# Kernel optimization log

Measured on AMD Instinct MI355X. Metric: run time of the kernel, lower is better.

Reference implementation:

```python
import jax, jax.numpy as jnp
import numpy as np

SCALE = 1.0 / np.sqrt(128.0).astype(np.float32)  # 1/sqrt(head_dim)


def setup_inputs() -> dict:
    key = jax.random.key(0)
    kq, kk, kv = jax.random.split(key, 3)
    B, S, D = 32, 2048, 128
    q = jax.random.normal(kq, (B, S, D), dtype=jnp.float32)
    k = jax.random.normal(kk, (B, S, D), dtype=jnp.float32)
    v = jax.random.normal(kv, (B, S, D), dtype=jnp.float32)
    return {"q": q, "k": k, "v": v}


def reference(q, k, v):
    # attention = bmm(q, k^T) * scale ; softmax over last (key) dim; bmm with v
    scores = jnp.einsum("bsd,btd->bst", q, k) * SCALE  # [B, S, S]
    attn = jax.nn.softmax(scores, axis=-1)
    return jnp.einsum("bst,btd->bsd", attn, v)  # [B, S, D]
```

## Files before the change

### kernel.cpp

```cpp
#include <hip/hip_runtime.h>
#include <math.h>
#include <stdint.h>

typedef __bf16 bf16_t;
typedef __bf16 bf16x2 __attribute__((ext_vector_type(2)));
typedef __bf16 bf16x4 __attribute__((ext_vector_type(4)));
typedef __bf16 bf16x8 __attribute__((ext_vector_type(8)));
typedef float f32x4 __attribute__((ext_vector_type(4)));
typedef float f32x16 __attribute__((ext_vector_type(16)));

#define NB   32
#define SEQ  2048
#define HD   128
#define SCALE 0.08838834764831845f
#define LOG2E 1.4426950408889634f

__device__ __forceinline__ float fast_exp2(float x) {
#if __has_builtin(__builtin_amdgcn_exp2f)
  return __builtin_amdgcn_exp2f(x);
#else
  return exp2f(x);
#endif
}

__global__ __launch_bounds__(256) void prep_kernel(
    const float* __restrict__ Q, const float* __restrict__ K,
    const float* __restrict__ V, bf16_t* __restrict__ Qs,
    bf16_t* __restrict__ Kb, bf16_t* __restrict__ Vt)
{
  const int b = blockIdx.x;
  const int tid = threadIdx.x;
  if (b < 4096) {
    const bool isQ = (b < 2048);
    const float* src = isQ ? Q : K;
    bf16_t* dst = isQ ? Qs : Kb;
    const float sc = isQ ? (SCALE * LOG2E) : 1.0f;
    size_t base4 = (size_t)(isQ ? b : b - 2048) * 1024;
#pragma unroll
    for (int i = 0; i < 4; ++i) {
      size_t idx = base4 + tid + i * 256;
      float4 x = ((const float4*)src)[idx];
      bf16x4 y;
      y[0] = (bf16_t)(x.x * sc); y[1] = (bf16_t)(x.y * sc);
      y[2] = (bf16_t)(x.z * sc); y[3] = (bf16_t)(x.w * sc);
      ((bf16x4*)dst)[idx] = y;
    }
  } else {
    __shared__ float tile[64][65];
    const int bt = b - 4096;
    const int batch = bt >> 6;
    const int rem = bt & 63;
    const int s0 = (rem >> 1) * 64;
    const int d0 = (rem & 1) * 64;
#pragma unroll
    for (int i = 0; i < 4; ++i) {
      int e = tid + i * 256;
      int s = e >> 4, dq = e & 15;
      float4 x = *(const float4*)&V[((size_t)batch * SEQ + s0 + s) * HD + d0 + dq * 4];
      tile[s][dq * 4 + 0] = x.x;
      tile[s][dq * 4 + 1] = x.y;
      tile[s][dq * 4 + 2] = x.z;
      tile[s][dq * 4 + 3] = x.w;
    }
    __syncthreads();
#pragma unroll
    for (int i = 0; i < 2; ++i) {
      int g = tid + i * 256;
      int d = g >> 3, sg = g & 7;
      bf16x8 w;
#pragma unroll
      for (int j = 0; j < 8; ++j) w[j] = (bf16_t)tile[sg * 8 + j][d];
      *(bf16x8*)&Vt[((size_t)batch * HD + d0 + d) * SEQ + s0 + sg * 8] = w;
    }
  }
}

__global__ __launch_bounds__(512, 4) void fa13_kernel(
    const bf16_t* __restrict__ Qs, const bf16_t* __restrict__ Kbf,
    const bf16_t* __restrict__ Vt, float* __restrict__ O)
{
  __shared__ __attribute__((aligned(16))) char smem[68608];
  bf16_t* const Ksw = (bf16_t*)smem;
  bf16_t* const Vsw = (bf16_t*)(smem + 32768);

  const int tid  = threadIdx.x;
  const int lane = tid & 63;
  const int wq   = tid >> 6;
  const int hi   = lane >> 5;
  const int q31  = lane & 31;
  const int pair = wq >> 1;
  const int sub  = wq & 1;
  const int koff = sub * 32;

  const int batch = blockIdx.x >> 4;
  const int qt    = blockIdx.x & 15;

  const bf16_t* Qb = Qs + ((size_t)batch * SEQ + qt * 128 + pair * 32) * HD;
  const bf16_t* Kb = Kbf + (size_t)batch * SEQ * HD;
  const bf16_t* Vb = Vt + (size_t)batch * HD * SEQ;
  float*        Ob = O + ((size_t)batch * SEQ + qt * 128) * HD;

  bf16x8 bq[8];
#pragma unroll
  for (int dc = 0; dc < 8; ++dc)
    bq[dc] = *(const bf16x8*)&Qb[(size_t)q31 * HD + dc * 16 + hi * 8];

  f32x16 o[4];
#pragma unroll
  for (int dt = 0; dt < 4; ++dt)
#pragma unroll
    for (int r = 0; r < 16; ++r) o[dt][r] = 0.f;
  float m_r = -INFINITY, l_r = 0.0f;

  auto stage = [&](int buf, int kb) {
#pragma unroll
    for (int i = 0; i < 2; ++i) {
      int row = wq * 8 + i * 4 + (lane >> 4);
      int gk = (lane & 15) ^ (row & 15);
      const bf16_t* gp = Kb + (size_t)(kb + row) * HD + gk * 8;
      __builtin_amdgcn_global_load_lds(
          (const __attribute__((address_space(1))) void*)gp,
          (__attribute__((address_space(3))) void*)&Ksw[buf * 8192 + (wq * 8 + i * 4) * 128],
          16, 0, 0);
    }
#pragma unroll
    for (int i = 0; i < 2; ++i) {
      int d = wq * 16 + i * 8 + (lane >> 3);
      int gv = (lane & 7) ^ (d & 7);
      const bf16_t* gp = Vb + (size_t)d * SEQ + kb + gv * 8;
      __builtin_amdgcn_global_load_lds(
          (const __attribute__((address_space(1))) void*)gp,
          (__attribute__((address_space(3))) void*)&Vsw[buf * 8192 + (wq * 16 + i * 8) * 64],
          16, 0, 0);
    }
  };

  stage(0, 0);

  for (int t = 0; t < SEQ / 64; ++t) {
    __syncthreads();
    if (t + 1 < SEQ / 64) stage((t + 1) & 1, (t + 1) * 64);

    const bf16_t* Ks = &Ksw[(t & 1) * 8192];
    const bf16_t* Vs = &Vsw[(t & 1) * 8192];

    f32x16 s;
#pragma unroll
    for (int r = 0; r < 16; ++r) s[r] = 0.f;
    {
      const int row = koff + q31;
      const int rsw = row & 15;
#pragma unroll
      for (int dc = 0; dc < 8; ++dc) {
        bf16x8 ak = *(const bf16x8*)&Ks[row * 128 + (((dc * 2 + hi) ^ rsw) * 8)];
        s = __builtin_amdgcn_mfma_f32_32x32x16_bf16(ak, bq[dc], s, 0, 0, 0);
      }
    }

    float mx = s[0];
#pragma unroll
    for (int r = 1; r < 16; ++r) mx = fmaxf(mx, s[r]);
    mx = fmaxf(mx, __shfl_xor(mx, 32));

    if (!__all(mx <= m_r + 8.0f)) {
      const float mnew = fmaxf(m_r, mx);
      const float alpha = fast_exp2(m_r - mnew);
      m_r = mnew;
      l_r *= alpha;
#pragma unroll
      for (int dt = 0; dt < 4; ++dt) o[dt] = o[dt] * alpha;
    }

    float ls = 0.f;
#pragma unroll
    for (int r = 0; r < 16; ++r) {
      float p = fast_exp2(s[r] - m_r);
      s[r] = p; ls += p;
    }
    ls += __shfl_xor(ls, 32);
    l_r += ls;

    uint32_t pk[8];
#pragma unroll
    for (int i = 0; i < 8; ++i) {
      union { bf16x2 v; uint32_t u; } c;
      c.v[0] = (bf16_t)s[2 * i];
      c.v[1] = (bf16_t)s[2 * i + 1];
      pk[i] = c.u;
    }
    uint32_t t0 = __shfl_xor((int)(hi ? pk[0] : pk[2]), 32);
    uint32_t t1 = __shfl_xor((int)(hi ? pk[1] : pk[3]), 32);
    uint32_t t2 = __shfl_xor((int)(hi ? pk[4] : pk[6]), 32);
    uint32_t t3 = __shfl_xor((int)(hi ? pk[5] : pk[7]), 32);
    bf16x8 bp0, bp1;
    {
      union { bf16x8 v; uint32_t w[4]; } B;
      if (hi) { B.w[0] = t0; B.w[1] = t1; B.w[2] = pk[2]; B.w[3] = pk[3]; }
      else    { B.w[0] = pk[0]; B.w[1] = pk[1]; B.w[2] = t0; B.w[3] = t1; }
      bp0 = B.v;
      if (hi) { B.w[0] = t2; B.w[1] = t3; B.w[2] = pk[6]; B.w[3] = pk[7]; }
      else    { B.w[0] = pk[4]; B.w[1] = pk[5]; B.w[2] = t2; B.w[3] = t3; }
      bp1 = B.v;
    }

    {
      const int g0 = (koff >> 3) + hi;
      const int g1 = g0 + 2;
#pragma unroll
      for (int dt = 0; dt < 4; ++dt) {
        const int d = dt * 32 + q31;
        const int dsw = d & 7;
        bf16x8 av0 = *(const bf16x8*)&Vs[d * 64 + ((g0 ^ dsw) * 8)];
        o[dt] = __builtin_amdgcn_mfma_f32_32x32x16_bf16(av0, bp0, o[dt], 0, 0, 0);
        bf16x8 av1 = *(const bf16x8*)&Vs[d * 64 + ((g1 ^ dsw) * 8)];
        o[dt] = __builtin_amdgcn_mfma_f32_32x32x16_bf16(av1, bp1, o[dt], 0, 0, 0);
      }
    }
  }

  __syncthreads();
  float* const sf  = (float*)smem;
  float* const mlb = (float*)(smem + 67584);

  if (sub == 1) {
    if (hi == 0) {
      mlb[pair * 64 + q31]      = m_r;
      mlb[pair * 64 + 32 + q31] = l_r;
    }
#pragma unroll
    for (int dt = 0; dt < 4; ++dt)
#pragma unroll
      for (int r = 0; r < 16; ++r) {
        int d = dt * 32 + (r & 3) + 8 * (r >> 2) + 4 * hi;
        sf[pair * 4224 + q31 * 132 + d] = o[dt][r];
      }
  }
  __syncthreads();
  if (sub == 0) {
    float m1 = mlb[pair * 64 + q31];
    float l1 = mlb[pair * 64 + 32 + q31];
    float m = fmaxf(m_r, m1);
    float e0 = fast_exp2(m_r - m);
    float e1 = fast_exp2(m1 - m);
    float inv = 1.0f / (l_r * e0 + l1 * e1);
    float f0 = e0 * inv, f1 = e1 * inv;
#pragma unroll
    for (int dt = 0; dt < 4; ++dt)
#pragma unroll
      for (int r = 0; r < 16; ++r) {
        int d = dt * 32 + (r & 3) + 8 * (r >> 2) + 4 * hi;
        float* p = &sf[pair * 4224 + q31 * 132 + d];
        *p = o[dt][r] * f0 + *p * f1;
      }
  }
  __syncthreads();
  {
#pragma unroll
    for (int i = 0; i < 8; ++i) {
      int idx = tid + i * 512;
      int q = idx >> 5;
      int dg = idx & 31;
      float4 v = *(const float4*)&sf[(q >> 5) * 4224 + (q & 31) * 132 + dg * 4];
      *(float4*)&Ob[(size_t)q * HD + dg * 4] = v;
    }
  }
}

#define BM   64
#define BN   64
#define KPAD 8
#define VPAD 8
#define PPAD 8

__global__ __launch_bounds__(256) void fa_fallback(
    const float* __restrict__ Q, const float* __restrict__ K,
    const float* __restrict__ V, float* __restrict__ O)
{
  __shared__ __attribute__((aligned(16))) bf16_t Ksh[BN][HD + KPAD];
  __shared__ __attribute__((aligned(16))) bf16_t Vsh[HD][BN + VPAD];
  __shared__ __attribute__((aligned(16))) bf16_t Psh[4][16][BN + PPAD];

  const int tid = threadIdx.x;
  const int lane = tid & 63;
  const int wq = tid >> 6;
  const int quad = lane >> 4;
  const int l15 = lane & 15;
  const int bid = blockIdx.x;
  const int batch = bid >> 5;
  const int qt = bid & 31;

  const float* Qb = Q + (size_t)batch * SEQ * HD + (size_t)qt * BM * HD;
  const float* Kb = K + (size_t)batch * SEQ * HD;
  const float* Vb = V + (size_t)batch * SEQ * HD;
  float* Ob = O + (size_t)batch * SEQ * HD + (size_t)qt * BM * HD;

  bf16x8 aq[4];
  {
    const int qrow = wq * 16 + l15;
#pragma unroll
    for (int kf = 0; kf < 4; ++kf) {
      const float* qp = Qb + (size_t)qrow * HD + kf * 32 + quad * 8;
      float4 x0 = *(const float4*)(qp);
      float4 x1 = *(const float4*)(qp + 4);
      bf16x8 a;
      a[0] = (bf16_t)(x0.x * SCALE); a[1] = (bf16_t)(x0.y * SCALE);
      a[2] = (bf16_t)(x0.z * SCALE); a[3] = (bf16_t)(x0.w * SCALE);
      a[4] = (bf16_t)(x1.x * SCALE); a[5] = (bf16_t)(x1.y * SCALE);
      a[6] = (bf16_t)(x1.z * SCALE); a[7] = (bf16_t)(x1.w * SCALE);
      aq[kf] = a;
    }
  }

  f32x4 o[8];
#pragma unroll
  for (int t = 0; t < 8; ++t) { o[t][0]=0.f; o[t][1]=0.f; o[t][2]=0.f; o[t][3]=0.f; }
  float m_r = -INFINITY, l_r = 0.0f;
  const int vkp = (tid & 31) * 2;
  const int vg = tid >> 5;
  float4 kreg[8], vreg[8];

#pragma unroll
  for (int i = 0; i < 8; ++i) {
    int v = tid + i * 256, row = v >> 5, c4 = (v & 31) * 4;
    kreg[i] = *(const float4*)(Kb + (size_t)row * HD + c4);
  }
#pragma unroll
  for (int i = 0; i < 4; ++i) {
    int d0 = (vg + i * 8) * 4;
    const float* vp0 = Vb + (size_t)vkp * HD + d0;
    vreg[2 * i] = *(const float4*)vp0;
    vreg[2 * i + 1] = *(const float4*)(vp0 + HD);
  }

  for (int kb = 0; kb < SEQ; kb += BN) {
    __syncthreads();
#pragma unroll
    for (int i = 0; i < 8; ++i) {
      int v = tid + i * 256, row = v >> 5, c4 = (v & 31) * 4;
      float4 kv = kreg[i];
      bf16x4 kk;
      kk[0]=(bf16_t)kv.x; kk[1]=(bf16_t)kv.y; kk[2]=(bf16_t)kv.z; kk[3]=(bf16_t)kv.w;
      *(bf16x4*)&Ksh[row][c4] = kk;
    }
#pragma unroll
    for (int i = 0; i < 4; ++i) {
      int d0 = (vg + i * 8) * 4;
      float4 a0 = vreg[2 * i], a1 = vreg[2 * i + 1];
      bf16x2 p0; p0[0]=(bf16_t)a0.x; p0[1]=(bf16_t)a1.x;
      bf16x2 p1; p1[0]=(bf16_t)a0.y; p1[1]=(bf16_t)a1.y;
      bf16x2 p2; p2[0]=(bf16_t)a0.z; p2[1]=(bf16_t)a1.z;
      bf16x2 p3; p3[0]=(bf16_t)a0.w; p3[1]=(bf16_t)a1.w;
      *(bf16x2*)&Vsh[d0 + 0][vkp] = p0;
      *(bf16x2*)&Vsh[d0 + 1][vkp] = p1;
      *(bf16x2*)&Vsh[d0 + 2][vkp] = p2;
      *(bf16x2*)&Vsh[d0 + 3][vkp] = p3;
    }
    __syncthreads();

    const int kbn = kb + BN;
    if (kbn < SEQ) {
#pragma unroll
      for (int i = 0; i < 8; ++i) {
        int v = tid + i * 256, row = v >> 5, c4 = (v & 31) * 4;
        kreg[i] = *(const float4*)(Kb + (size_t)(kbn + row) * HD + c4);
      }
#pragma unroll
      for (int i = 0; i < 4; ++i) {
        int d0 = (vg + i * 8) * 4;
        const float* vp0 = Vb + (size_t)(kbn + vkp) * HD + d0;
        vreg[2 * i] = *(const float4*)vp0;
        vreg[2 * i + 1] = *(const float4*)(vp0 + HD);
      }
    }

    f32x4 s[4];
#pragma unroll
    for (int ct = 0; ct < 4; ++ct) { s[ct][0]=0.f; s[ct][1]=0.f; s[ct][2]=0.f; s[ct][3]=0.f; }
#pragma unroll
    for (int kf = 0; kf < 4; ++kf)
#pragma unroll
      for (int ct = 0; ct < 4; ++ct) {
        bf16x8 ak = *(const bf16x8*)&Ksh[ct * 16 + l15][kf * 32 + quad * 8];
        s[ct] = __builtin_amdgcn_mfma_f32_16x16x32_bf16(ak, aq[kf], s[ct], 0, 0, 0);
      }

    float mx = s[0][0];
#pragma unroll
    for (int ct = 0; ct < 4; ++ct)
#pragma unroll
      for (int r = 0; r < 4; ++r) mx = fmaxf(mx, s[ct][r]);
    mx = fmaxf(mx, __shfl_xor(mx, 16));
    mx = fmaxf(mx, __shfl_xor(mx, 32));
    float mnew = fmaxf(m_r, mx);
    float alpha = __expf(m_r - mnew);
    m_r = mnew;
    float ls = 0.f;
#pragma unroll
    for (int ct = 0; ct < 4; ++ct)
#pragma unroll
      for (int r = 0; r < 4; ++r) {
        float p = __expf(s[ct][r] - mnew);
        s[ct][r] = p; ls += p;
      }
    ls += __shfl_xor(ls, 16);
    ls += __shfl_xor(ls, 32);
    l_r = l_r * alpha + ls;

#pragma unroll
    for (int ct = 0; ct < 4; ++ct) {
      bf16x4 pp;
      pp[0]=(bf16_t)s[ct][0]; pp[1]=(bf16_t)s[ct][1];
      pp[2]=(bf16_t)s[ct][2]; pp[3]=(bf16_t)s[ct][3];
      *(bf16x4*)&Psh[wq][l15][ct * 16 + quad * 4] = pp;
    }
    asm volatile("s_waitcnt lgkmcnt(0)" ::: "memory");
    bf16x8 ap0 = *(const bf16x8*)&Psh[wq][l15][quad * 8];
    bf16x8 ap1 = *(const bf16x8*)&Psh[wq][l15][32 + quad * 8];

#pragma unroll
    for (int t = 0; t < 8; ++t) {
      o[t][0]*=alpha; o[t][1]*=alpha; o[t][2]*=alpha; o[t][3]*=alpha;
    }
#pragma unroll
    for (int t = 0; t < 8; ++t) {
      bf16x8 av0 = *(const bf16x8*)&Vsh[t * 16 + l15][quad * 8];
      o[t] = __builtin_amdgcn_mfma_f32_16x16x32_bf16(av0, ap0, o[t], 0, 0, 0);
      bf16x8 av1 = *(const bf16x8*)&Vsh[t * 16 + l15][32 + quad * 8];
      o[t] = __builtin_amdgcn_mfma_f32_16x16x32_bf16(av1, ap1, o[t], 0, 0, 0);
    }
  }

  float inv = 1.0f / l_r;
  const int qrow = wq * 16 + l15;
#pragma unroll
  for (int t = 0; t < 8; ++t) {
    float4 w;
    w.x = o[t][0]*inv; w.y = o[t][1]*inv; w.z = o[t][2]*inv; w.w = o[t][3]*inv;
    *(float4*)&Ob[(size_t)qrow * HD + t * 16 + quad * 4] = w;
  }
}

extern "C" void kernel_launch(void* const* d_in, const int* in_sizes, int n_in,
                              void* d_out, int out_size, void* d_ws, size_t ws_size,
                              hipStream_t stream) {
  const float* q = (const float*)d_in[0];
  const float* k = (const float*)d_in[1];
  const float* v = (const float*)d_in[2];
  float* out = (float*)d_out;

  const size_t elems = (size_t)NB * SEQ * HD;
  const size_t need = elems * 2 * 3;

  if (ws_size >= need) {
    bf16_t* Qs = (bf16_t*)d_ws;
    bf16_t* Kb = Qs + elems;
    bf16_t* Vt = Kb + elems;
    prep_kernel<<<6144, 256, 0, stream>>>(q, k, v, Qs, Kb, Vt);
    fa13_kernel<<<NB * (SEQ / 128), 512, 0, stream>>>(Qs, Kb, Vt, out);
  } else {
    fa_fallback<<<NB * (SEQ / BM), 256, 0, stream>>>(q, k, v, out);
  }
}
```

Baseline: 270.2 us.

## Software-pipeline PV matmul one tile behind QK with triple-buffered V, smaller blocks

Defers each tile's P·V MFMA to the next iteration so it runs alongside the following tile's Q·K^T, which needs a third V buffer in LDS. Blocks shrink from 512 to 256 threads covering 64 query rows, and each thread now stages twice as many K/V chunks. Block indices are remapped so that consecutive blocks are spread across batches, likely to balance work over XCDs/L2. The aim is to hide the softmax dependency latency and improve MFMA overlap, at the cost of more LDS per block (80KB), which may lower occupancy, and twice the K/V traffic per query row.

```diff
diff --git a/kernel.cpp b/kernel.cpp
--- a/kernel.cpp
+++ b/kernel.cpp
@@ -75,11 +75,11 @@
   }
 }
 
-__global__ __launch_bounds__(512, 4) void fa13_kernel(
+__global__ __launch_bounds__(256) void fa14_kernel(
     const bf16_t* __restrict__ Qs, const bf16_t* __restrict__ Kbf,
     const bf16_t* __restrict__ Vt, float* __restrict__ O)
 {
-  __shared__ __attribute__((aligned(16))) char smem[68608];
+  __shared__ __attribute__((aligned(16))) char smem[81920];
   bf16_t* const Ksw = (bf16_t*)smem;
   bf16_t* const Vsw = (bf16_t*)(smem + 32768);
 
@@ -92,13 +92,14 @@
   const int sub  = wq & 1;
   const int koff = sub * 32;
 
-  const int batch = blockIdx.x >> 4;
-  const int qt    = blockIdx.x & 15;
-
-  const bf16_t* Qb = Qs + ((size_t)batch * SEQ + qt * 128 + pair * 32) * HD;
+  const int L     = ((blockIdx.x & 7) << 7) | (blockIdx.x >> 3);
+  const int batch = L >> 5;
+  const int qt    = L & 31;
+
+  const bf16_t* Qb = Qs + ((size_t)batch * SEQ + qt * 64 + pair * 32) * HD;
   const bf16_t* Kb = Kbf + (size_t)batch * SEQ * HD;
   const bf16_t* Vb = Vt + (size_t)batch * HD * SEQ;
-  float*        Ob = O + ((size_t)batch * SEQ + qt * 128) * HD;
+  float*        Ob = O + ((size_t)batch * SEQ + qt * 64) * HD;
 
   bf16x8 bq[8];
 #pragma unroll
@@ -112,37 +113,40 @@
     for (int r = 0; r < 16; ++r) o[dt][r] = 0.f;
   float m_r = -INFINITY, l_r = 0.0f;
 
-  auto stage = [&](int buf, int kb) {
-#pragma unroll
-    for (int i = 0; i < 2; ++i) {
-      int row = wq * 8 + i * 4 + (lane >> 4);
+  bf16x8 bp0p, bp1p;
+
+  auto stage = [&](int kbuf, int vbuf, int kb) {
+#pragma unroll
+    for (int i = 0; i < 4; ++i) {
+      int row = wq * 16 + i * 4 + (lane >> 4);
       int gk = (lane & 15) ^ (row & 15);
       const bf16_t* gp = Kb + (size_t)(kb + row) * HD + gk * 8;
       __builtin_amdgcn_global_load_lds(
           (const __attribute__((address_space(1))) void*)gp,
-          (__attribute__((address_space(3))) void*)&Ksw[buf * 8192 + (wq * 8 + i * 4) * 128],
+          (__attribute__((address_space(3))) void*)&Ksw[kbuf * 8192 + (wq * 16 + i * 4) * 128],
           16, 0, 0);
     }
 #pragma unroll
-    for (int i = 0; i < 2; ++i) {
-      int d = wq * 16 + i * 8 + (lane >> 3);
+    for (int i = 0; i < 4; ++i) {
+      int d = wq * 32 + i * 8 + (lane >> 3);
       int gv = (lane & 7) ^ (d & 7);
       const bf16_t* gp = Vb + (size_t)d * SEQ + kb + gv * 8;
       __builtin_amdgcn_global_load_lds(
           (const __attribute__((address_space(1))) void*)gp,
-          (__attribute__((address_space(3))) void*)&Vsw[buf * 8192 + (wq * 16 + i * 8) * 64],
+          (__attribute__((address_space(3))) void*)&Vsw[vbuf * 8192 + (wq * 32 + i * 8) * 64],
           16, 0, 0);
     }
   };
 
-  stage(0, 0);
+  stage(0, 0, 0);
 
   for (int t = 0; t < SEQ / 64; ++t) {
     __syncthreads();
-    if (t + 1 < SEQ / 64) stage((t + 1) & 1, (t + 1) * 64);
+    const int vnext = (t + 1) % 3;
+    const int vprev = (t + 2) % 3;
+    if (t + 1 < SEQ / 64) stage((t + 1) & 1, vnext, (t + 1) * 64);
 
     const bf16_t* Ks = &Ksw[(t & 1) * 8192];
-    const bf16_t* Vs = &Vsw[(t & 1) * 8192];
 
     f32x16 s;
 #pragma unroll
@@ -154,6 +158,21 @@
       for (int dc = 0; dc < 8; ++dc) {
         bf16x8 ak = *(const bf16x8*)&Ks[row * 128 + (((dc * 2 + hi) ^ rsw) * 8)];
         s = __builtin_amdgcn_mfma_f32_32x32x16_bf16(ak, bq[dc], s, 0, 0, 0);
+      }
+    }
+
+    if (t > 0) {
+      const bf16_t* Vp = &Vsw[vprev * 8192];
+      const int g0 = (koff >> 3) + hi;
+      const int g1 = g0 + 2;
+#pragma unroll
+      for (int dt = 0; dt < 4; ++dt) {
+        const int d = dt * 32 + q31;
+        const int dsw = d & 7;
+        bf16x8 av0 = *(const bf16x8*)&Vp[d * 64 + ((g0 ^ dsw) * 8)];
+        o[dt] = __builtin_amdgcn_mfma_f32_32x32x16_bf16(av0, bp0p, o[dt], 0, 0, 0);
+        bf16x8 av1 = *(const bf16x8*)&Vp[d * 64 + ((g1 ^ dsw) * 8)];
+        o[dt] = __builtin_amdgcn_mfma_f32_32x32x16_bf16(av1, bp1p, o[dt], 0, 0, 0);
       }
     }
 
@@ -192,35 +211,35 @@
     uint32_t t1 = __shfl_xor((int)(hi ? pk[1] : pk[3]), 32);
     uint32_t t2 = __shfl_xor((int)(hi ? pk[4] : pk[6]), 32);
     uint32_t t3 = __shfl_xor((int)(hi ? pk[5] : pk[7]), 32);
-    bf16x8 bp0, bp1;
     {
       union { bf16x8 v; uint32_t w[4]; } B;
       if (hi) { B.w[0] = t0; B.w[1] = t1; B.w[2] = pk[2]; B.w[3] = pk[3]; }
       else    { B.w[0] = pk[0]; B.w[1] = pk[1]; B.w[2] = t0; B.w[3] = t1; }
-      bp0 = B.v;
+      bp0p = B.v;
       if (hi) { B.w[0] = t2; B.w[1] = t3; B.w[2] = pk[6]; B.w[3] = pk[7]; }
       else    { B.w[0] = pk[4]; B.w[1] = pk[5]; B.w[2] = t2; B.w[3] = t3; }
-      bp1 = B.v;
-    }
-
-    {
-      const int g0 = (koff >> 3) + hi;
-      const int g1 = g0 + 2;
-#pragma unroll
-      for (int dt = 0; dt < 4; ++dt) {
-        const int d = dt * 32 + q31;
-        const int dsw = d & 7;
-        bf16x8 av0 = *(const bf16x8*)&Vs[d * 64 + ((g0 ^ dsw) * 8)];
-        o[dt] = __builtin_amdgcn_mfma_f32_32x32x16_bf16(av0, bp0, o[dt], 0, 0, 0);
-        bf16x8 av1 = *(const bf16x8*)&Vs[d * 64 + ((g1 ^ dsw) * 8)];
-        o[dt] = __builtin_amdgcn_mfma_f32_32x32x16_bf16(av1, bp1, o[dt], 0, 0, 0);
-      }
+      bp1p = B.v;
+    }
+  }
+
+  {
+    const bf16_t* Vp = &Vsw[((SEQ / 64 - 1) % 3) * 8192];
+    const int g0 = (koff >> 3) + hi;
+    const int g1 = g0 + 2;
+#pragma unroll
+    for (int dt = 0; dt < 4; ++dt) {
+      const int d = dt * 32 + q31;
+      const int dsw = d & 7;
+      bf16x8 av0 = *(const bf16x8*)&Vp[d * 64 + ((g0 ^ dsw) * 8)];
+      o[dt] = __builtin_amdgcn_mfma_f32_32x32x16_bf16(av0, bp0p, o[dt], 0, 0, 0);
+      bf16x8 av1 = *(const bf16x8*)&Vp[d * 64 + ((g1 ^ dsw) * 8)];
+      o[dt] = __builtin_amdgcn_mfma_f32_32x32x16_bf16(av1, bp1p, o[dt], 0, 0, 0);
     }
   }
 
   __syncthreads();
   float* const sf  = (float*)smem;
-  float* const mlb = (float*)(smem + 67584);
+  float* const mlb = (float*)(smem + 33792);
 
   if (sub == 1) {
     if (hi == 0) {
@@ -255,13 +274,14 @@
   }
   __syncthreads();
   {
+    const int tid2 = sub * 64 + lane;
 #pragma unroll
     for (int i = 0; i < 8; ++i) {
-      int idx = tid + i * 512;
+      int idx = tid2 + i * 128;
       int q = idx >> 5;
       int dg = idx & 31;
-      float4 v = *(const float4*)&sf[(q >> 5) * 4224 + (q & 31) * 132 + dg * 4];
-      *(float4*)&Ob[(size_t)q * HD + dg * 4] = v;
+      float4 v = *(const float4*)&sf[pair * 4224 + q * 132 + dg * 4];
+      *(float4*)&Ob[(size_t)(pair * 32 + q) * HD + dg * 4] = v;
     }
   }
 }
@@ -456,7 +476,7 @@
     bf16_t* Kb = Qs + elems;
     bf16_t* Vt = Kb + elems;
     prep_kernel<<<6144, 256, 0, stream>>>(q, k, v, Qs, Kb, Vt);
-    fa13_kernel<<<NB * (SEQ / 128), 512, 0, stream>>>(Qs, Kb, Vt, out);
+    fa14_kernel<<<NB * (SEQ / 64), 256, 0, stream>>>(Qs, Kb, Vt, out);
   } else {
     fa_fallback<<<NB * (SEQ / BM), 256, 0, stream>>>(q, k, v, out);
   }
```

New measurement: 232.3 us. 1.16x faster.
